# Kernel optimization log

Hardware: AMD Instinct MI355X
Metric: run time of the kernel (lower is better)

## Reference

```python
import jax, jax.numpy as jnp
import numpy as np

DIM = 256
HEADS = 4
HEAD_DIM = DIM // HEADS
SCALE = HEAD_DIM ** -0.5


def setup_inputs() -> dict:
    key = jax.random.key(0)
    ks = jax.random.split(key, 6)
    B, N, C = 4, 4096, DIM
    x = jax.random.normal(ks[0], (B, N, C), dtype=jnp.float32)
    # torch.nn.Linear weights are [out, in]; y = x @ W.T (+ b)
    s = 1.0 / np.sqrt(C)
    Wq = jax.random.uniform(ks[1], (C, C), jnp.float32, -s, s)
    Wk = jax.random.uniform(ks[2], (C, C), jnp.float32, -s, s)
    Wv = jax.random.uniform(ks[3], (C, C), jnp.float32, -s, s)
    Wp = jax.random.uniform(ks[4], (C, C), jnp.float32, -s, s)
    bp = jax.random.uniform(ks[5], (C,), jnp.float32, -s, s)
    return {"x": x, "Wq": Wq, "Wk": Wk, "Wv": Wv, "Wp": Wp, "bp": bp}


def reference(x, Wq, Wk, Wv, Wp, bp):
    B, N, C = x.shape
    H, D = HEADS, HEAD_DIM
    # project and split heads: [B, H, N, D]
    def heads(W):
        return (x @ W.T).reshape(B, N, H, D).transpose(0, 2, 1, 3)
    q = heads(Wq)
    k = heads(Wk)
    v = heads(Wv)
    attn = jnp.einsum('bhnd,bhmd->bhnm', q, k) * SCALE  # [B,H,N,N]
    attn = jax.nn.softmax(attn, axis=-1)
    out = jnp.einsum('bhnm,bhmd->bhnd', attn, v)  # [B,H,N,D]
    out = out.transpose(0, 2, 1, 3).reshape(B, N, C)
    return out @ Wp.T + bp
```

## Files before the change

kernel.cpp:

```cpp
#include <hip/hip_runtime.h>

typedef unsigned short u16t;
typedef unsigned int u32t;
typedef __bf16 bf16x8 __attribute__((ext_vector_type(8)));
typedef float f32x4 __attribute__((ext_vector_type(4)));
typedef float f32x16 __attribute__((ext_vector_type(16)));
typedef unsigned int u32x4 __attribute__((ext_vector_type(4)));
typedef unsigned int u32x2 __attribute__((ext_vector_type(2)));

#define DEV static __device__ __forceinline__

DEV u16t f2bf(float f){
  u32t u = __builtin_bit_cast(u32t, f);
  u += 0x7fffu + ((u >> 16) & 1u);
  return (u16t)(u >> 16);
}

DEV u32t cvtpk(float lo, float hi){
  u32t r;
  asm("v_cvt_pk_bf16_f32 %0, %1, %2" : "=v"(r) : "v"(lo), "v"(hi));
  return r;
}

DEV void plswap(u32t &a, u32t &b){
  asm("v_permlane32_swap_b32 %0, %1" : "+v"(a), "+v"(b));
}

DEV float fexp2(float x){
#if __has_builtin(__builtin_amdgcn_exp2f)
  return __builtin_amdgcn_exp2f(x);
#else
  return exp2f(x);
#endif
}

DEV void gll16(const void* g, void* l){
  __builtin_amdgcn_global_load_lds((const __attribute__((address_space(1))) void*)g,
                                   (__attribute__((address_space(3))) void*)l, 16, 0, 0);
}

DEV f32x4 mfma16(bf16x8 a, bf16x8 b, f32x4 c){
  return __builtin_amdgcn_mfma_f32_16x16x32_bf16(a, b, c, 0, 0, 0);
}

DEV f32x16 mfma32(bf16x8 a, bf16x8 b, f32x16 c){
  return __builtin_amdgcn_mfma_f32_32x32x16_bf16(a, b, c, 0, 0, 0);
}

__global__ __launch_bounds__(256) void k_cast_x(const float4* __restrict__ x, u16t* __restrict__ xb){
  int idx = blockIdx.x * 256 + threadIdx.x;
  float4 v = x[idx];
  ushort4 o = make_ushort4(f2bf(v.x), f2bf(v.y), f2bf(v.z), f2bf(v.w));
  *(ushort4*)&xb[idx * 4] = o;
}

__global__ __launch_bounds__(256) void k_cast_w(const float* __restrict__ Wq, const float* __restrict__ Wk,
                         const float* __restrict__ Wv, const float* __restrict__ Wp,
                         u16t* __restrict__ wqkv, u16t* __restrict__ wp){
  int idx = blockIdx.x * 256 + threadIdx.x;
  if (idx < 196608){
    float v;
    if (idx < 65536)        v = Wq[idx] * 0.1803368801f;
    else if (idx < 131072)  v = Wk[idx - 65536];
    else                    v = Wv[idx - 131072];
    wqkv[idx] = f2bf(v);
  } else {
    int j = idx - 196608;
    wp[j] = f2bf(Wp[j]);
  }
}

template<bool IS_QKV>
__global__ __launch_bounds__(256) void k_gemm(const u16t* __restrict__ A, const u16t* __restrict__ W,
    const float* __restrict__ bias, u16t* __restrict__ oq, u16t* __restrict__ okk, u16t* __restrict__ vtg,
    float* __restrict__ op, int Ntot){
  __shared__ u32x4 sm[1536];
  const int tid = threadIdx.x, lane = tid & 63, w = tid >> 6, g = lane >> 4, li = lane & 15;
  const int m0 = blockIdx.x * 128, n0 = blockIdx.y * 64;
  const int wm = w >> 1, wn = w & 1;
  f32x4 acc[4][2] = {};
  for (int kk = 0; kk < 4; ++kk){
    #pragma unroll
    for (int rnd = 0; rnd < 4; ++rnd){
      int cid = rnd * 256 + tid;
      int row = cid >> 3, ch = cid & 7;
      const u16t* src = A + (m0 + row) * 256 + kk * 64 + ((ch ^ (row & 7)) << 3);
      gll16(src, (char*)sm + (rnd * 256 + w * 64) * 16);
    }
    #pragma unroll
    for (int rnd = 0; rnd < 2; ++rnd){
      int cid = rnd * 256 + tid;
      int row = cid >> 3, ch = cid & 7;
      const u16t* src = W + (n0 + row) * 256 + kk * 64 + ((ch ^ (row & 7)) << 3);
      gll16(src, (char*)sm + 16384 + (rnd * 256 + w * 64) * 16);
    }
    __syncthreads();
    #pragma unroll
    for (int ks = 0; ks < 2; ++ks){
      bf16x8 bfr[2];
      #pragma unroll
      for (int nj = 0; nj < 2; ++nj){
        int row = wn * 32 + nj * 16 + li;
        bfr[nj] = __builtin_bit_cast(bf16x8, sm[1024 + row * 8 + ((ks * 4 + g) ^ (row & 7))]);
      }
      #pragma unroll
      for (int mi = 0; mi < 4; ++mi){
        int row = wm * 64 + mi * 16 + li;
        bf16x8 af = __builtin_bit_cast(bf16x8, sm[row * 8 + ((ks * 4 + g) ^ (row & 7))]);
        #pragma unroll
        for (int nj = 0; nj < 2; ++nj)
          acc[mi][nj] = mfma16(af, bfr[nj], acc[mi][nj]);
      }
    }
    __syncthreads();
  }
  if (IS_QKV){
    const int which = n0 >> 8, h = (n0 >> 6) & 3;
    if (which == 2){
      u16t* smv = (u16t*)sm;
      #pragma unroll
      for (int mi = 0; mi < 4; ++mi){
        #pragma unroll
        for (int nj = 0; nj < 2; ++nj){
          int d = wn * 32 + nj * 16 + li;
          int mloc = wm * 64 + mi * 16 + g * 4;
          u32x2 pk2;
          pk2.x = cvtpk(acc[mi][nj][0], acc[mi][nj][1]);
          pk2.y = cvtpk(acc[mi][nj][2], acc[mi][nj][3]);
          int chk = mloc >> 3, inner = (mloc & 7) * 2;
          *(u32x2*)((char*)smv + d * 256 + (((chk ^ (d & 7))) << 4) + inner) = pk2;
        }
      }
      __syncthreads();
      const int b = m0 >> 12, bh2 = b * 4 + h, mbase = m0 & 4095;
      #pragma unroll
      for (int rnd = 0; rnd < 4; ++rnd){
        int qq = rnd * 256 + tid;
        int d = qq >> 4, ch = qq & 15;
        *(u32x4*)&vtg[((size_t)bh2 * 64 + d) * 4096 + mbase + ch * 8] =
            *(const u32x4*)((char*)smv + d * 256 + ((ch ^ (d & 7)) << 4));
      }
    } else {
      u16t* outp = which == 0 ? oq : okk;
      #pragma unroll
      for (int mi = 0; mi < 4; ++mi){
        int m = m0 + wm * 64 + mi * 16 + g * 4;
        int b = m >> 12, nn = m & 4095;
        #pragma unroll
        for (int nj = 0; nj < 2; ++nj){
          int d = wn * 32 + nj * 16 + li;
          #pragma unroll
          for (int r = 0; r < 4; ++r)
            outp[((b * 4 + h) * 4096 + nn + r) * 64 + d] = f2bf(acc[mi][nj][r]);
        }
      }
    }
  } else {
    #pragma unroll
    for (int mi = 0; mi < 4; ++mi){
      int m = m0 + wm * 64 + mi * 16 + g * 4;
      #pragma unroll
      for (int nj = 0; nj < 2; ++nj){
        int n = n0 + wn * 32 + nj * 16 + li;
        float bv = bias[n];
        #pragma unroll
        for (int r = 0; r < 4; ++r)
          op[(m + r) * Ntot + n] = acc[mi][nj][r] + bv;
      }
    }
  }
}

__global__ __launch_bounds__(128, 1) void k_flash(const u16t* __restrict__ q,
    const u16t* __restrict__ kg, const u16t* __restrict__ vtg, u16t* __restrict__ ao){
  __shared__ char sm[49152];
  const int tid = threadIdx.x, lane = tid & 63, w = tid >> 6;
  const int hi = lane >> 5, p = lane & 31;
  const int bid = blockIdx.x;
  const int swz = (bid & 7) * 64 + (bid >> 3);
  const int bh = swz >> 5, qt = swz & 31;
  const int rowbase = qt * 128 + w * 64;
  const u16t* kb = kg + (size_t)bh * 262144;
  const u16t* vb = vtg + (size_t)bh * 262144;

  u32x4 qf[2][4];
  #pragma unroll
  for (int it = 0; it < 2; ++it)
    #pragma unroll
    for (int kk = 0; kk < 4; ++kk)
      qf[it][kk] = *(const u32x4*)&q[((size_t)bh * 4096 + rowbase + it * 32 + p) * 64 + kk * 16 + hi * 8];

  f32x16 ot[2][2] = {};
  float lsp[2][4] = {};

  auto stage = [&](int t, int c){
    #pragma unroll
    for (int rnd = 0; rnd < 4; ++rnd){
      int cid = rnd * 128 + tid;
      int row = cid >> 3, ch = cid & 7;
      gll16(kb + (t * 64 + row) * 64 + ((ch ^ (row & 7)) << 3), sm + c * 8192 + cid * 16);
      gll16(vb + row * 4096 + t * 64 + ((ch ^ (row & 7)) << 3), sm + 24576 + c * 8192 + cid * 16);
    }
  };

  auto compute = [&](int cbuf){
    const char* kbuf = sm + cbuf * 8192;
    const char* vbuf = sm + 24576 + cbuf * 8192;
    f32x16 st[2][2] = {};
    #pragma unroll
    for (int kk = 0; kk < 4; ++kk)
      #pragma unroll
      for (int jt = 0; jt < 2; ++jt){
        int row = jt * 32 + p;
        bf16x8 kf = __builtin_bit_cast(bf16x8,
            *(const u32x4*)(kbuf + row * 128 + (((kk * 2 + hi) ^ (row & 7)) << 4)));
        st[0][jt] = mfma32(kf, __builtin_bit_cast(bf16x8, qf[0][kk]), st[0][jt]);
        st[1][jt] = mfma32(kf, __builtin_bit_cast(bf16x8, qf[1][kk]), st[1][jt]);
      }
    u32x4 pf[2][2][2];
    #pragma unroll
    for (int it = 0; it < 2; ++it)
      #pragma unroll
      for (int jt = 0; jt < 2; ++jt){
        float e[16];
        #pragma unroll
        for (int r = 0; r < 16; ++r)
          e[r] = fexp2(st[it][jt][r]);
        #pragma unroll
        for (int r = 0; r < 16; ++r)
          lsp[it][r & 3] += e[r];
        #pragma unroll
        for (int s = 0; s < 2; ++s){
          u32t a0 = cvtpk(e[s*8+0], e[s*8+1]);
          u32t a1 = cvtpk(e[s*8+2], e[s*8+3]);
          u32t b0 = cvtpk(e[s*8+4], e[s*8+5]);
          u32t b1 = cvtpk(e[s*8+6], e[s*8+7]);
          plswap(a0, b0);
          plswap(a1, b1);
          pf[it][jt][s] = (u32x4){a0, a1, b0, b1};
        }
      }
    #pragma unroll
    for (int jt = 0; jt < 2; ++jt)
      #pragma unroll
      for (int s = 0; s < 2; ++s)
        #pragma unroll
        for (int dt = 0; dt < 2; ++dt){
          int row = dt * 32 + p;
          bf16x8 vf = __builtin_bit_cast(bf16x8,
              *(const u32x4*)(vbuf + row * 128 + ((((jt * 2 + s) * 2 + hi) ^ (row & 7)) << 4)));
          ot[0][dt] = mfma32(vf, __builtin_bit_cast(bf16x8, pf[0][jt][s]), ot[0][dt]);
          ot[1][dt] = mfma32(vf, __builtin_bit_cast(bf16x8, pf[1][jt][s]), ot[1][dt]);
        }
  };

  stage(0, 0);
  stage(1, 1);
  int c = 0;
  #pragma unroll 1
  for (int t = 0; t < 63; ++t){
    asm volatile("s_waitcnt vmcnt(8)" ::: "memory");
    __builtin_amdgcn_s_barrier();
    asm volatile("" ::: "memory");
    int nb = c + 2; if (nb > 2) nb -= 3;
    if (t < 62) stage(t + 2, nb);
    compute(c);
    c = (c == 2) ? 0 : c + 1;
  }
  asm volatile("s_waitcnt vmcnt(0)" ::: "memory");
  __builtin_amdgcn_s_barrier();
  asm volatile("" ::: "memory");
  compute(c);
  __syncthreads();

  float inv[2];
  #pragma unroll
  for (int it = 0; it < 2; ++it){
    float l4 = (lsp[it][0] + lsp[it][1]) + (lsp[it][2] + lsp[it][3]);
    l4 += __shfl_xor(l4, 32);
    inv[it] = __builtin_amdgcn_rcpf(l4);
  }
  char* smw = sm + w * 8192;
  #pragma unroll
  for (int it = 0; it < 2; ++it)
    #pragma unroll
    for (int dt = 0; dt < 2; ++dt)
      #pragma unroll
      for (int k2 = 0; k2 < 8; ++k2){
        int d0 = ((2*k2) & 3) + 8 * ((2*k2) >> 2) + 4 * hi + dt * 32;
        u32t pk = cvtpk(ot[it][dt][2*k2] * inv[it], ot[it][dt][2*k2+1] * inv[it]);
        int row = it * 32 + p;
        int colb = d0 * 2;
        *(u32t*)(smw + row * 128 + (((colb >> 4) ^ (row & 7)) << 4) + (colb & 15)) = pk;
      }
  const int b = bh >> 2, h = bh & 3;
  #pragma unroll
  for (int rnd = 0; rnd < 8; ++rnd){
    int qq = rnd * 64 + lane;
    int row = qq >> 3, ch = qq & 7;
    u32x4 v = *(const u32x4*)(smw + row * 128 + ((ch ^ (row & 7)) << 4));
    *(u32x4*)&ao[((size_t)b * 4096 + rowbase + row) * 256 + h * 64 + ch * 8] = v;
  }
}

extern "C" void kernel_launch(void* const* d_in, const int* in_sizes, int n_in,
                              void* d_out, int out_size, void* d_ws, size_t ws_size,
                              hipStream_t stream){
  (void)in_sizes; (void)n_in; (void)out_size; (void)ws_size;
  const float* x  = (const float*)d_in[0];
  const float* Wq = (const float*)d_in[1];
  const float* Wk = (const float*)d_in[2];
  const float* Wv = (const float*)d_in[3];
  const float* Wp = (const float*)d_in[4];
  const float* bp = (const float*)d_in[5];
  float* out = (float*)d_out;

  u16t* ws   = (u16t*)d_ws;
  u16t* xb   = ws;
  u16t* qg   = ws + 4194304;
  u16t* kg   = ws + 8388608;
  u16t* vtg  = ws + 12582912;
  u16t* ao   = ws + 16777216;
  u16t* wqkv = ws + 20971520;
  u16t* wpb  = ws + 21168128;

  k_cast_x<<<4096, 256, 0, stream>>>((const float4*)x, xb);
  k_cast_w<<<1024, 256, 0, stream>>>(Wq, Wk, Wv, Wp, wqkv, wpb);
  k_gemm<true><<<dim3(128, 12), 256, 0, stream>>>(xb, wqkv, nullptr, qg, kg, vtg, nullptr, 768);
  k_flash<<<512, 128, 0, stream>>>(qg, kg, vtg, ao);
  k_gemm<false><<<dim3(128, 4), 256, 0, stream>>>(ao, wpb, bp, nullptr, nullptr, nullptr, out, 256);
}
```

Measured before the change: 113.9 us.

## Split KV range across waves in flash kernel and double block count

Each 128-thread block now owns 64 query rows, and its two waves each process half of the key/value sequence. Every wave has private single-buffered K and V LDS tiles refilled asynchronously without block barriers. Partial outputs and row sums are combined through LDS at the end. LDS per block is smaller and launch bounds allow two blocks per CU, doubling the grid to raise occupancy and latency hiding. The cost is an extra cross-wave reduction, a redundant wrapped prefetch on the last iteration, and less prefetch depth per wave.

```diff
diff --git a/kernel.cpp b/kernel.cpp
--- a/kernel.cpp
+++ b/kernel.cpp
@@ -171,17 +171,20 @@
   }
 }
 
-__global__ __launch_bounds__(128, 1) void k_flash(const u16t* __restrict__ q,
+__global__ __launch_bounds__(128, 2) void k_flash(const u16t* __restrict__ q,
     const u16t* __restrict__ kg, const u16t* __restrict__ vtg, u16t* __restrict__ ao){
-  __shared__ char sm[49152];
+  __shared__ u32x4 sm4[2080];
+  char* sm = (char*)sm4;
   const int tid = threadIdx.x, lane = tid & 63, w = tid >> 6;
   const int hi = lane >> 5, p = lane & 31;
   const int bid = blockIdx.x;
-  const int swz = (bid & 7) * 64 + (bid >> 3);
-  const int bh = swz >> 5, qt = swz & 31;
-  const int rowbase = qt * 128 + w * 64;
-  const u16t* kb = kg + (size_t)bh * 262144;
-  const u16t* vb = vtg + (size_t)bh * 262144;
+  const int swz = (bid & 7) * 128 + (bid >> 3);
+  const int bh = swz >> 6, qt = swz & 63;
+  const int rowbase = qt * 64;
+  const u16t* kb = kg + (size_t)bh * 262144 + (size_t)w * 2048 * 64;
+  const u16t* vb = vtg + (size_t)bh * 262144 + w * 2048;
+  char* Kb = sm + w * 16384;
+  char* Vb = Kb + 8192;
 
   u32x4 qf[2][4];
   #pragma unroll
@@ -193,19 +196,28 @@
   f32x16 ot[2][2] = {};
   float lsp[2][4] = {};
 
-  auto stage = [&](int t, int c){
-    #pragma unroll
-    for (int rnd = 0; rnd < 4; ++rnd){
-      int cid = rnd * 128 + tid;
+  auto stageK = [&](int t){
+    #pragma unroll
+    for (int i = 0; i < 8; ++i){
+      int cid = i * 64 + lane;
       int row = cid >> 3, ch = cid & 7;
-      gll16(kb + (t * 64 + row) * 64 + ((ch ^ (row & 7)) << 3), sm + c * 8192 + cid * 16);
-      gll16(vb + row * 4096 + t * 64 + ((ch ^ (row & 7)) << 3), sm + 24576 + c * 8192 + cid * 16);
+      gll16(kb + (t * 64 + row) * 64 + ((ch ^ (row & 7)) << 3), Kb + cid * 16);
     }
   };
-
-  auto compute = [&](int cbuf){
-    const char* kbuf = sm + cbuf * 8192;
-    const char* vbuf = sm + 24576 + cbuf * 8192;
+  auto stageV = [&](int t){
+    #pragma unroll
+    for (int i = 0; i < 8; ++i){
+      int cid = i * 64 + lane;
+      int row = cid >> 3, ch = cid & 7;
+      gll16(vb + row * 4096 + t * 64 + ((ch ^ (row & 7)) << 3), Vb + cid * 16);
+    }
+  };
+
+  stageK(0);
+  stageV(0);
+  #pragma unroll 1
+  for (int t = 0; t < 32; ++t){
+    asm volatile("s_waitcnt vmcnt(8)" ::: "memory");
     f32x16 st[2][2] = {};
     #pragma unroll
     for (int kk = 0; kk < 4; ++kk)
@@ -213,10 +225,12 @@
       for (int jt = 0; jt < 2; ++jt){
         int row = jt * 32 + p;
         bf16x8 kf = __builtin_bit_cast(bf16x8,
-            *(const u32x4*)(kbuf + row * 128 + (((kk * 2 + hi) ^ (row & 7)) << 4)));
+            *(const u32x4*)(Kb + row * 128 + (((kk * 2 + hi) ^ (row & 7)) << 4)));
         st[0][jt] = mfma32(kf, __builtin_bit_cast(bf16x8, qf[0][kk]), st[0][jt]);
         st[1][jt] = mfma32(kf, __builtin_bit_cast(bf16x8, qf[1][kk]), st[1][jt]);
       }
+    asm volatile("s_waitcnt lgkmcnt(0)" ::: "memory");
+    stageK((t + 1) & 31);
     u32x4 pf[2][2][2];
     #pragma unroll
     for (int it = 0; it < 2; ++it)
@@ -240,6 +254,7 @@
           pf[it][jt][s] = (u32x4){a0, a1, b0, b1};
         }
       }
+    asm volatile("s_waitcnt vmcnt(8)" ::: "memory");
     #pragma unroll
     for (int jt = 0; jt < 2; ++jt)
       #pragma unroll
@@ -248,58 +263,61 @@
         for (int dt = 0; dt < 2; ++dt){
           int row = dt * 32 + p;
           bf16x8 vf = __builtin_bit_cast(bf16x8,
-              *(const u32x4*)(vbuf + row * 128 + ((((jt * 2 + s) * 2 + hi) ^ (row & 7)) << 4)));
+              *(const u32x4*)(Vb + row * 128 + ((((jt * 2 + s) * 2 + hi) ^ (row & 7)) << 4)));
           ot[0][dt] = mfma32(vf, __builtin_bit_cast(bf16x8, pf[0][jt][s]), ot[0][dt]);
           ot[1][dt] = mfma32(vf, __builtin_bit_cast(bf16x8, pf[1][jt][s]), ot[1][dt]);
         }
-  };
-
-  stage(0, 0);
-  stage(1, 1);
-  int c = 0;
-  #pragma unroll 1
-  for (int t = 0; t < 63; ++t){
-    asm volatile("s_waitcnt vmcnt(8)" ::: "memory");
-    __builtin_amdgcn_s_barrier();
-    asm volatile("" ::: "memory");
-    int nb = c + 2; if (nb > 2) nb -= 3;
-    if (t < 62) stage(t + 2, nb);
-    compute(c);
-    c = (c == 2) ? 0 : c + 1;
-  }
-  asm volatile("s_waitcnt vmcnt(0)" ::: "memory");
-  __builtin_amdgcn_s_barrier();
-  asm volatile("" ::: "memory");
-  compute(c);
-  __syncthreads();
-
-  float inv[2];
+    asm volatile("s_waitcnt lgkmcnt(0)" ::: "memory");
+    stageV((t + 1) & 31);
+  }
+  asm volatile("s_waitcnt vmcnt(0) lgkmcnt(0)" ::: "memory");
+
+  float l4[2];
   #pragma unroll
   for (int it = 0; it < 2; ++it){
-    float l4 = (lsp[it][0] + lsp[it][1]) + (lsp[it][2] + lsp[it][3]);
-    l4 += __shfl_xor(l4, 32);
-    inv[it] = __builtin_amdgcn_rcpf(l4);
-  }
-  char* smw = sm + w * 8192;
+    float v = (lsp[it][0] + lsp[it][1]) + (lsp[it][2] + lsp[it][3]);
+    v += __shfl_xor(v, 32);
+    l4[it] = v;
+  }
+  __syncthreads();
+
+  char* reg = sm + w * 16384;
   #pragma unroll
   for (int it = 0; it < 2; ++it)
     #pragma unroll
     for (int dt = 0; dt < 2; ++dt)
       #pragma unroll
-      for (int k2 = 0; k2 < 8; ++k2){
-        int d0 = ((2*k2) & 3) + 8 * ((2*k2) >> 2) + 4 * hi + dt * 32;
-        u32t pk = cvtpk(ot[it][dt][2*k2] * inv[it], ot[it][dt][2*k2+1] * inv[it]);
-        int row = it * 32 + p;
-        int colb = d0 * 2;
-        *(u32t*)(smw + row * 128 + (((colb >> 4) ^ (row & 7)) << 4) + (colb & 15)) = pk;
-      }
-  const int b = bh >> 2, h = bh & 3;
-  #pragma unroll
-  for (int rnd = 0; rnd < 8; ++rnd){
-    int qq = rnd * 64 + lane;
-    int row = qq >> 3, ch = qq & 7;
-    u32x4 v = *(const u32x4*)(smw + row * 128 + ((ch ^ (row & 7)) << 4));
-    *(u32x4*)&ao[((size_t)b * 4096 + rowbase + row) * 256 + h * 64 + ch * 8] = v;
+      for (int s = 0; s < 4; ++s){
+        f32x4 v4 = {ot[it][dt][4*s+0], ot[it][dt][4*s+1], ot[it][dt][4*s+2], ot[it][dt][4*s+3]};
+        int quad = 2 * s + hi + 8 * dt;
+        *(f32x4*)(reg + it * 8192 + p * 256 + ((quad ^ (p & 15)) << 4)) = v4;
+      }
+  float* lsums = (float*)(sm + 32768);
+  if (lane < 32){
+    lsums[(w * 2 + 0) * 32 + lane] = l4[0];
+    lsums[(w * 2 + 1) * 32 + lane] = l4[1];
+  }
+  __syncthreads();
+
+  {
+    const int qloc = lane >> 1, dh = lane & 1;
+    float ltot = lsums[(0 * 2 + w) * 32 + qloc] + lsums[(1 * 2 + w) * 32 + qloc];
+    float inv = __builtin_amdgcn_rcpf(ltot);
+    const int b = bh >> 2, h = bh & 3;
+    u16t* dst = ao + ((size_t)b * 4096 + rowbase + w * 32 + qloc) * 256 + h * 64 + dh * 32;
+    u32t pk[16];
+    #pragma unroll
+    for (int k = 0; k < 8; ++k){
+      int quad = dh * 8 + k;
+      f32x4 a = *(const f32x4*)(sm + 0 * 16384 + w * 8192 + qloc * 256 + ((quad ^ (qloc & 15)) << 4));
+      f32x4 c = *(const f32x4*)(sm + 1 * 16384 + w * 8192 + qloc * 256 + ((quad ^ (qloc & 15)) << 4));
+      f32x4 o = (a + c) * inv;
+      pk[2*k]   = cvtpk(o[0], o[1]);
+      pk[2*k+1] = cvtpk(o[2], o[3]);
+    }
+    #pragma unroll
+    for (int k = 0; k < 4; ++k)
+      *(u32x4*)(dst + k * 8) = (u32x4){pk[4*k], pk[4*k+1], pk[4*k+2], pk[4*k+3]};
   }
 }
 
@@ -327,6 +345,6 @@
   k_cast_x<<<4096, 256, 0, stream>>>((const float4*)x, xb);
   k_cast_w<<<1024, 256, 0, stream>>>(Wq, Wk, Wv, Wp, wqkv, wpb);
   k_gemm<true><<<dim3(128, 12), 256, 0, stream>>>(xb, wqkv, nullptr, qg, kg, vtg, nullptr, 768);
-  k_flash<<<512, 128, 0, stream>>>(qg, kg, vtg, ao);
+  k_flash<<<1024, 128, 0, stream>>>(qg, kg, vtg, ao);
   k_gemm<false><<<dim3(128, 4), 256, 0, stream>>>(ao, wpb, bp, nullptr, nullptr, nullptr, out, 256);
 }
```

After: 111.5 us. -2.1%, faster.

## Pre-swizzle K/V into fragment-order tiles and use 4 waves of 32 rows

Applied to the files above, without the earlier changes.

The QKV GEMM epilogue now writes K and V^T in a tile layout that matches the MFMA fragment order. The flash kernel can then stage each tile with contiguous per-thread 16-byte loads and read LDS fragments without XOR swizzle math. The flash block goes from 2 waves of 64 query rows to 4 waves of 32 rows, and the triple buffer becomes a double buffer with an extra barrier per iteration. This cuts register pressure and address arithmetic, but each wave now reuses each K/V tile over fewer rows, and the extra sync may expose load latency.

```diff
diff --git a/kernel.cpp b/kernel.cpp
--- a/kernel.cpp
+++ b/kernel.cpp
@@ -136,12 +136,30 @@
       #pragma unroll
       for (int rnd = 0; rnd < 4; ++rnd){
         int qq = rnd * 256 + tid;
-        int d = qq >> 4, ch = qq & 15;
-        *(u32x4*)&vtg[((size_t)bh2 * 64 + d) * 4096 + mbase + ch * 8] =
-            *(const u32x4*)((char*)smv + d * 256 + ((ch ^ (d & 7)) << 4));
+        int d = qq & 63, cidx = qq >> 6;
+        u32x4 val = *(const u32x4*)((char*)smv + d * 256 + ((cidx ^ (d & 7)) << 4));
+        int nt = (mbase >> 6) + (cidx >> 3), i = cidx & 7;
+        *(u32x4*)((char*)vtg + ((((size_t)bh2 * 64 + nt) * 8 + i) * 64 + d) * 16) = val;
+      }
+    } else if (which == 1){
+      #pragma unroll
+      for (int mi = 0; mi < 4; ++mi){
+        int m = m0 + wm * 64 + mi * 16 + g * 4;
+        int b = m >> 12;
+        #pragma unroll
+        for (int nj = 0; nj < 2; ++nj){
+          int d = wn * 32 + nj * 16 + li;
+          int kk2 = d >> 4, dhi = (d >> 3) & 1, e = d & 7;
+          #pragma unroll
+          for (int r = 0; r < 4; ++r){
+            int row = (m + r) & 4095;
+            int nt = row >> 6, jt = (row >> 5) & 1, pp = row & 31;
+            okk[(size_t)(b * 4 + h) * 262144 + nt * 4096 + (kk2 * 2 + jt) * 512 + dhi * 256 + pp * 8 + e]
+              = f2bf(acc[mi][nj][r]);
+          }
+        }
       }
     } else {
-      u16t* outp = which == 0 ? oq : okk;
       #pragma unroll
       for (int mi = 0; mi < 4; ++mi){
         int m = m0 + wm * 64 + mi * 16 + g * 4;
@@ -151,7 +169,7 @@
           int d = wn * 32 + nj * 16 + li;
           #pragma unroll
           for (int r = 0; r < 4; ++r)
-            outp[((b * 4 + h) * 4096 + nn + r) * 64 + d] = f2bf(acc[mi][nj][r]);
+            oq[((b * 4 + h) * 4096 + nn + r) * 64 + d] = f2bf(acc[mi][nj][r]);
         }
       }
     }
@@ -171,135 +189,119 @@
   }
 }
 
-__global__ __launch_bounds__(128, 1) void k_flash(const u16t* __restrict__ q,
-    const u16t* __restrict__ kg, const u16t* __restrict__ vtg, u16t* __restrict__ ao){
-  __shared__ char sm[49152];
+__global__ __launch_bounds__(256) void k_flash(const u16t* __restrict__ q,
+    const u16t* __restrict__ kslot, const u16t* __restrict__ vslot, u16t* __restrict__ ao){
+  __shared__ char sm[32768];
   const int tid = threadIdx.x, lane = tid & 63, w = tid >> 6;
   const int hi = lane >> 5, p = lane & 31;
   const int bid = blockIdx.x;
   const int swz = (bid & 7) * 64 + (bid >> 3);
   const int bh = swz >> 5, qt = swz & 31;
-  const int rowbase = qt * 128 + w * 64;
-  const u16t* kb = kg + (size_t)bh * 262144;
-  const u16t* vb = vtg + (size_t)bh * 262144;
-
-  u32x4 qf[2][4];
+  const int rowbase = qt * 128 + w * 32;
+  const char* kbB = (const char*)kslot + (size_t)bh * 524288 + tid * 16;
+  const char* vbB = (const char*)vslot + (size_t)bh * 524288 + tid * 16;
+
+  auto stage = [&](int t, int c){
+    char* dst = sm + c * 16384 + tid * 16;
+    const char* sK = kbB + (size_t)t * 8192;
+    const char* sV = vbB + (size_t)t * 8192;
+    gll16(sK, dst);
+    gll16(sK + 4096, dst + 4096);
+    gll16(sV, dst + 8192);
+    gll16(sV + 4096, dst + 12288);
+  };
+
+  u32x4 qf[4];
   #pragma unroll
-  for (int it = 0; it < 2; ++it)
-    #pragma unroll
-    for (int kk = 0; kk < 4; ++kk)
-      qf[it][kk] = *(const u32x4*)&q[((size_t)bh * 4096 + rowbase + it * 32 + p) * 64 + kk * 16 + hi * 8];
-
-  f32x16 ot[2][2] = {};
-  float lsp[2][4] = {};
-
-  auto stage = [&](int t, int c){
-    #pragma unroll
-    for (int rnd = 0; rnd < 4; ++rnd){
-      int cid = rnd * 128 + tid;
-      int row = cid >> 3, ch = cid & 7;
-      gll16(kb + (t * 64 + row) * 64 + ((ch ^ (row & 7)) << 3), sm + c * 8192 + cid * 16);
-      gll16(vb + row * 4096 + t * 64 + ((ch ^ (row & 7)) << 3), sm + 24576 + c * 8192 + cid * 16);
-    }
-  };
-
-  auto compute = [&](int cbuf){
-    const char* kbuf = sm + cbuf * 8192;
-    const char* vbuf = sm + 24576 + cbuf * 8192;
-    f32x16 st[2][2] = {};
-    #pragma unroll
-    for (int kk = 0; kk < 4; ++kk)
-      #pragma unroll
-      for (int jt = 0; jt < 2; ++jt){
-        int row = jt * 32 + p;
-        bf16x8 kf = __builtin_bit_cast(bf16x8,
-            *(const u32x4*)(kbuf + row * 128 + (((kk * 2 + hi) ^ (row & 7)) << 4)));
-        st[0][jt] = mfma32(kf, __builtin_bit_cast(bf16x8, qf[0][kk]), st[0][jt]);
-        st[1][jt] = mfma32(kf, __builtin_bit_cast(bf16x8, qf[1][kk]), st[1][jt]);
-      }
-    u32x4 pf[2][2][2];
-    #pragma unroll
-    for (int it = 0; it < 2; ++it)
-      #pragma unroll
-      for (int jt = 0; jt < 2; ++jt){
-        float e[16];
-        #pragma unroll
-        for (int r = 0; r < 16; ++r)
-          e[r] = fexp2(st[it][jt][r]);
-        #pragma unroll
-        for (int r = 0; r < 16; ++r)
-          lsp[it][r & 3] += e[r];
-        #pragma unroll
-        for (int s = 0; s < 2; ++s){
-          u32t a0 = cvtpk(e[s*8+0], e[s*8+1]);
-          u32t a1 = cvtpk(e[s*8+2], e[s*8+3]);
-          u32t b0 = cvtpk(e[s*8+4], e[s*8+5]);
-          u32t b1 = cvtpk(e[s*8+6], e[s*8+7]);
-          plswap(a0, b0);
-          plswap(a1, b1);
-          pf[it][jt][s] = (u32x4){a0, a1, b0, b1};
-        }
-      }
-    #pragma unroll
-    for (int jt = 0; jt < 2; ++jt)
-      #pragma unroll
-      for (int s = 0; s < 2; ++s)
-        #pragma unroll
-        for (int dt = 0; dt < 2; ++dt){
-          int row = dt * 32 + p;
-          bf16x8 vf = __builtin_bit_cast(bf16x8,
-              *(const u32x4*)(vbuf + row * 128 + ((((jt * 2 + s) * 2 + hi) ^ (row & 7)) << 4)));
-          ot[0][dt] = mfma32(vf, __builtin_bit_cast(bf16x8, pf[0][jt][s]), ot[0][dt]);
-          ot[1][dt] = mfma32(vf, __builtin_bit_cast(bf16x8, pf[1][jt][s]), ot[1][dt]);
-        }
-  };
-
+  for (int kk = 0; kk < 4; ++kk)
+    qf[kk] = *(const u32x4*)&q[((size_t)bh * 4096 + rowbase + p) * 64 + kk * 16 + hi * 8];
+  asm volatile("s_waitcnt vmcnt(0)" ::: "memory");
   stage(0, 0);
   stage(1, 1);
-  int c = 0;
+
+  f32x16 ot[2] = {};
+  float lsp[4] = {};
+  const f32x16 fz = {};
+
   #pragma unroll 1
-  for (int t = 0; t < 63; ++t){
-    asm volatile("s_waitcnt vmcnt(8)" ::: "memory");
+  for (int t = 0; t < 64; ++t){
+    asm volatile("s_waitcnt vmcnt(4)" ::: "memory");
     __builtin_amdgcn_s_barrier();
     asm volatile("" ::: "memory");
-    int nb = c + 2; if (nb > 2) nb -= 3;
-    if (t < 62) stage(t + 2, nb);
-    compute(c);
-    c = (c == 2) ? 0 : c + 1;
+    const char* Kb = sm + (t & 1) * 16384;
+    const char* Vt = Kb + 8192;
+    f32x16 st[2];
+    #pragma unroll
+    for (int kk = 0; kk < 4; ++kk)
+      #pragma unroll
+      for (int jt = 0; jt < 2; ++jt){
+        bf16x8 kf = __builtin_bit_cast(bf16x8,
+            *(const u32x4*)(Kb + (kk * 2 + jt) * 1024 + lane * 16));
+        st[jt] = mfma32(kf, __builtin_bit_cast(bf16x8, qf[kk]), kk == 0 ? fz : st[jt]);
+      }
+    #pragma unroll
+    for (int jt = 0; jt < 2; ++jt){
+      float e[16];
+      #pragma unroll
+      for (int r = 0; r < 16; ++r)
+        e[r] = fexp2(st[jt][r]);
+      #pragma unroll
+      for (int r = 0; r < 16; ++r)
+        lsp[r & 3] += e[r];
+      u32x4 pf[2];
+      #pragma unroll
+      for (int s = 0; s < 2; ++s){
+        u32t a0 = cvtpk(e[s*8+0], e[s*8+1]);
+        u32t a1 = cvtpk(e[s*8+2], e[s*8+3]);
+        u32t b0 = cvtpk(e[s*8+4], e[s*8+5]);
+        u32t b1 = cvtpk(e[s*8+6], e[s*8+7]);
+        plswap(a0, b0);
+        plswap(a1, b1);
+        pf[s] = (u32x4){a0, a1, b0, b1};
+      }
+      #pragma unroll
+      for (int s = 0; s < 2; ++s)
+        #pragma unroll
+        for (int dt = 0; dt < 2; ++dt){
+          bf16x8 vf = __builtin_bit_cast(bf16x8,
+              *(const u32x4*)(Vt + ((jt * 2 + s) * 2 + hi) * 1024 + dt * 512 + p * 16));
+          ot[dt] = mfma32(vf, __builtin_bit_cast(bf16x8, pf[s]), ot[dt]);
+        }
+    }
+    asm volatile("s_waitcnt lgkmcnt(0)" ::: "memory");
+    __builtin_amdgcn_s_barrier();
+    asm volatile("" ::: "memory");
+    stage((t + 2) & 63, t & 1);
   }
   asm volatile("s_waitcnt vmcnt(0)" ::: "memory");
   __builtin_amdgcn_s_barrier();
   asm volatile("" ::: "memory");
-  compute(c);
-  __syncthreads();
-
-  float inv[2];
+
+  float l = (lsp[0] + lsp[1]) + (lsp[2] + lsp[3]);
+  l += __shfl_xor(l, 32);
+  float inv = __builtin_amdgcn_rcpf(l);
+
+  char* reg = sm + w * 4096;
   #pragma unroll
-  for (int it = 0; it < 2; ++it){
-    float l4 = (lsp[it][0] + lsp[it][1]) + (lsp[it][2] + lsp[it][3]);
-    l4 += __shfl_xor(l4, 32);
-    inv[it] = __builtin_amdgcn_rcpf(l4);
-  }
-  char* smw = sm + w * 8192;
-  #pragma unroll
-  for (int it = 0; it < 2; ++it)
-    #pragma unroll
-    for (int dt = 0; dt < 2; ++dt)
-      #pragma unroll
-      for (int k2 = 0; k2 < 8; ++k2){
-        int d0 = ((2*k2) & 3) + 8 * ((2*k2) >> 2) + 4 * hi + dt * 32;
-        u32t pk = cvtpk(ot[it][dt][2*k2] * inv[it], ot[it][dt][2*k2+1] * inv[it]);
-        int row = it * 32 + p;
-        int colb = d0 * 2;
-        *(u32t*)(smw + row * 128 + (((colb >> 4) ^ (row & 7)) << 4) + (colb & 15)) = pk;
-      }
-  const int b = bh >> 2, h = bh & 3;
-  #pragma unroll
-  for (int rnd = 0; rnd < 8; ++rnd){
-    int qq = rnd * 64 + lane;
-    int row = qq >> 3, ch = qq & 7;
-    u32x4 v = *(const u32x4*)(smw + row * 128 + ((ch ^ (row & 7)) << 4));
-    *(u32x4*)&ao[((size_t)b * 4096 + rowbase + row) * 256 + h * 64 + ch * 8] = v;
+  for (int dt = 0; dt < 2; ++dt)
+    #pragma unroll
+    for (int k = 0; k < 8; ++k){
+      int d0 = ((2 * k) & 3) + 8 * (k >> 1) + 4 * hi + 32 * dt;
+      u32t pkv = cvtpk(ot[dt][2 * k] * inv, ot[dt][2 * k + 1] * inv);
+      int ch = d0 >> 3, inner = (d0 & 7) * 2;
+      *(u32t*)(reg + p * 128 + ((ch ^ (p & 7)) << 4) + inner) = pkv;
+    }
+  {
+    const int b = bh >> 2, h = bh & 3;
+    int row = lane >> 1, half = lane & 1;
+    const char* src = sm + w * 4096 + row * 128;
+    u16t* dst = ao + ((size_t)b * 4096 + rowbase + row) * 256 + h * 64 + half * 32;
+    #pragma unroll
+    for (int j = 0; j < 4; ++j){
+      int ch = half * 4 + j;
+      u32x4 v = *(const u32x4*)(src + ((ch ^ (row & 7)) << 4));
+      *(u32x4*)(dst + j * 8) = v;
+    }
   }
 }
 
@@ -327,6 +329,6 @@
   k_cast_x<<<4096, 256, 0, stream>>>((const float4*)x, xb);
   k_cast_w<<<1024, 256, 0, stream>>>(Wq, Wk, Wv, Wp, wqkv, wpb);
   k_gemm<true><<<dim3(128, 12), 256, 0, stream>>>(xb, wqkv, nullptr, qg, kg, vtg, nullptr, 768);
-  k_flash<<<512, 128, 0, stream>>>(qg, kg, vtg, ao);
+  k_flash<<<512, 256, 0, stream>>>(qg, kg, vtg, ao);
   k_gemm<false><<<dim3(128, 4), 256, 0, stream>>>(ao, wpb, bp, nullptr, nullptr, nullptr, out, 256);
 }
```

After: 122.1 us. +7.2%, slower.
